# Kernel optimization log

Measured on AMD Instinct MI355X. Metric: run time of the kernel, lower is better.

Reference implementation:

```python
import jax, jax.numpy as jnp
import numpy as np

B, N, D = 16, 512, 256   # batch, tokens(=input_size), emb_dim
H, DH = 8, 16            # heads, dim_head
INNER = H * DH           # 128
SCALE = DH ** -0.5
EPS = 1e-5


def _p(key, shape):
    return jax.random.normal(key, shape, dtype=jnp.float32) * 0.02


def setup_inputs() -> dict:
    key = jax.random.key(0)
    ks = jax.random.split(key, 12)
    inp = {
        "x": jax.random.normal(ks[0], (B, N, D), dtype=jnp.float32),
        # stage-1 attention (tokens=N, feat=D)
        "wqkv1": _p(ks[1], (D, 3 * INNER)),
        "wo1": _p(ks[2], (INNER, D)),
        "bo1": jnp.zeros((D,), jnp.float32),
        "ff1_w1": _p(ks[3], (D, 8 * D)),
        "ff1_b1": jnp.zeros((8 * D,), jnp.float32),
        "ff1_w2": _p(ks[4], (4 * D, D)),
        "ff1_b2": jnp.zeros((D,), jnp.float32),
        # stage-2 attention (tokens=D after transpose, feat=N=input_size)
        "wqkv2": _p(ks[5], (N, 3 * INNER)),
        "wo2": _p(ks[6], (INNER, N)),
        "bo2": jnp.zeros((N,), jnp.float32),
        "ff2_w1": _p(ks[7], (N, 8 * N)),
        "ff2_b1": jnp.zeros((8 * N,), jnp.float32),
        "ff2_w2": _p(ks[8], (4 * N, N)),
        "ff2_b2": jnp.zeros((N,), jnp.float32),
        # layernorms
        "ln1_g": jnp.ones((D,), jnp.float32), "ln1_b": jnp.zeros((D,), jnp.float32),
        "ln2_g": jnp.ones((D,), jnp.float32), "ln2_b": jnp.zeros((D,), jnp.float32),
        "ln3_g": jnp.ones((N,), jnp.float32), "ln3_b": jnp.zeros((N,), jnp.float32),
        "ln4_g": jnp.ones((N,), jnp.float32), "ln4_b": jnp.zeros((N,), jnp.float32),
    }
    return inp


def _layernorm(x, g, b):
    mu = jnp.mean(x, axis=-1, keepdims=True)
    var = jnp.mean(jnp.square(x - mu), axis=-1, keepdims=True)
    return (x - mu) * jax.lax.rsqrt(var + EPS) * g + b


def _attention(x, wqkv, wo, bo, share):
    b, n, _ = x.shape
    qkv = x @ wqkv                                 # [b, n, 3*INNER]
    q, k, v = jnp.split(qkv, 3, axis=-1)
    split_heads = lambda t: t.reshape(b, n, H, DH).transpose(0, 2, 1, 3)
    q, k, v = split_heads(q), split_heads(k), split_heads(v)
    energy = jnp.einsum('bhid,bhjd->bhij', q, k) * SCALE
    if share is not None:
        energy = energy + share
    attn = jax.nn.softmax(energy, axis=-1)
    out = jnp.einsum('bhij,bhjd->bhid', attn, v)   # [b, h, n, dh]
    out = out.transpose(0, 2, 1, 3).reshape(b, n, INNER)
    return out @ wo + bo, energy


def _geglu_ff(x, w1, b1, w2, b2):
    h = x @ w1 + b1
    a, g = jnp.split(h, 2, axis=-1)
    return (a * jax.nn.gelu(g, approximate=False)) @ w2 + b2


def reference(x, wqkv1, wo1, bo1, ff1_w1, ff1_b1, ff1_w2, ff1_b2,
              wqkv2, wo2, bo2, ff2_w1, ff2_b1, ff2_w2, ff2_b2,
              ln1_g, ln1_b, ln2_g, ln2_b, ln3_g, ln3_b, ln4_g, ln4_b):
    # stage 1: token attention + FFN
    attn_out, share = _attention(x, wqkv1, wo1, bo1, None)
    x = _layernorm(attn_out + x, ln1_g, ln1_b)
    x = _layernorm(_geglu_ff(x, ff1_w1, ff1_b1, ff1_w2, ff1_b2) + x, ln2_g, ln2_b)
    # stage 2: feature (column) attention + FFN on transposed x
    x = x.transpose(0, 2, 1)                       # [b, D, N]
    attn_out, share2 = _attention(x, wqkv2, wo2, bo2, None)
    x = _layernorm(attn_out + x, ln3_g, ln3_b)
    x = _layernorm(_geglu_ff(x, ff2_w1, ff2_b1, ff2_w2, ff2_b2) + x, ln4_g, ln4_b)
    x = x.transpose(0, 2, 1)                       # [b, N, D]
    return (x, share, share2)
```

## Files before the change

kernel.cpp:

```cpp
#include <hip/hip_runtime.h>
#include <cstddef>


typedef __attribute__((ext_vector_type(8))) short short8;
typedef __attribute__((ext_vector_type(4))) short bf16x4;
typedef __attribute__((ext_vector_type(4))) float f32x4;
typedef unsigned short u16t;

__device__ __forceinline__ u16t f2b(float f) {
  union { float f; unsigned u; } x; x.f = f;
  unsigned r = (x.u + 0x7fffu + ((x.u >> 16) & 1u)) >> 16;
  return (u16t)r;
}

__device__ __forceinline__ void gload16(const void* g, void* l) {
  __builtin_amdgcn_global_load_lds(
      (const __attribute__((address_space(1))) void*)g,
      (__attribute__((address_space(3))) void*)l, 16, 0, 0);
}

__device__ __forceinline__ float gelu_f(float g) {
  const float x = g * 0.70710678118654752f;
  const float ax = fabsf(x);
  const float t = 1.f / (1.f + 0.3275911f * ax);
  const float p = t * (0.254829592f + t * (-0.284496736f +
                  t * (1.421413741f + t * (-1.453152027f + t * 1.061405429f))));
  const float er = 1.f - p * __expf(-x * x);
  return 0.5f * g * (1.f + copysignf(er, x));
}

__device__ __forceinline__ int origcol(int n, int halfN) {
  const int nb = n >> 7, s = (n >> 4) & 7, r = n & 15;
  return ((s & 1) ? halfN : 0) + (nb << 6) + ((s >> 1) << 4) + r;
}

template<int EPI>
__global__ __launch_bounds__(256) void mgemm(
    const u16t* __restrict__ A, const u16t* __restrict__ BT,
    const float* __restrict__ bias, const float* __restrict__ res,
    void* __restrict__ C, int M, int N, int K) {
  __shared__ u16t Al[128 * 32];
  __shared__ u16t Bl[128 * 32];
  const int t = threadIdx.x, lane = t & 63, wid = t >> 6;
  const int wr = wid >> 1, wc = wid & 1;
  const int lr = lane & 15, lq = lane >> 4;
  const int bm = blockIdx.y << 7, bn = blockIdx.x << 7;

  const int ao0 = wid * 2048 + lane * 16;
  const int ar0 = ao0 >> 6,          ac0 = (ao0 & 63) >> 1;
  const int ar1 = (ao0 + 1024) >> 6, ac1 = ((ao0 + 1024) & 63) >> 1;

  const u16t* Ab = A + (size_t)bm * K;
  const u16t* Bb = BT + (size_t)bn * K;

  f32x4 acc[4][4];
#pragma unroll
  for (int m = 0; m < 4; ++m)
#pragma unroll
    for (int n = 0; n < 4; ++n) acc[m][n] = (f32x4){0.f, 0.f, 0.f, 0.f};

  for (int k0 = 0; k0 < K; k0 += 32) {
    gload16(Ab + (size_t)ar0 * K + k0 + ac0, (char*)Al + wid * 2048);
    gload16(Ab + (size_t)ar1 * K + k0 + ac1, (char*)Al + wid * 2048 + 1024);
    gload16(Bb + (size_t)ar0 * K + k0 + ac0, (char*)Bl + wid * 2048);
    gload16(Bb + (size_t)ar1 * K + k0 + ac1, (char*)Bl + wid * 2048 + 1024);
    __syncthreads();
    short8 af[4], bf[4];
#pragma unroll
    for (int m = 0; m < 4; ++m)
      af[m] = *(const short8*)&Al[(wr * 64 + m * 16 + lr) * 32 + lq * 8];
#pragma unroll
    for (int n = 0; n < 4; ++n)
      bf[n] = *(const short8*)&Bl[(wc * 64 + n * 16 + lr) * 32 + lq * 8];
#pragma unroll
    for (int m = 0; m < 4; ++m)
#pragma unroll
      for (int n = 0; n < 4; ++n)
        acc[m][n] = __builtin_amdgcn_mfma_f32_16x16x32_bf16(af[m], bf[n], acc[m][n], 0, 0, 0);
    __syncthreads();
  }

  if (EPI == 2) {
    const int Nh = N >> 1;
#pragma unroll
    for (int np = 0; np < 2; ++np) {
      const int ca = bn + wc * 64 + np * 32 + lr;
      const float ba = bias[ca], bg = bias[ca + 16];
      const int uc = (bn >> 1) + wc * 32 + np * 16 + lr;
#pragma unroll
      for (int m = 0; m < 4; ++m) {
#pragma unroll
        for (int i = 0; i < 4; ++i) {
          const int row = bm + wr * 64 + m * 16 + lq * 4 + i;
          const float a = acc[m][2 * np][i] + ba;
          const float g = acc[m][2 * np + 1][i] + bg;
          ((u16t*)C)[(size_t)row * Nh + uc] = f2b(a * gelu_f(g));
        }
      }
    }
  } else {
#pragma unroll
    for (int n = 0; n < 4; ++n) {
      const int col = bn + wc * 64 + n * 16 + lr;
      const float bv = bias ? bias[col] : 0.f;
#pragma unroll
      for (int m = 0; m < 4; ++m) {
#pragma unroll
        for (int i = 0; i < 4; ++i) {
          const int row = bm + wr * 64 + m * 16 + lq * 4 + i;
          float v = acc[m][n][i] + bv;
          if (EPI == 1) {
            v += res[(size_t)row * N + col];
            ((float*)C)[(size_t)row * N + col] = v;
          } else {
            ((u16t*)C)[(size_t)row * N + col] = f2b(v);
          }
        }
      }
    }
  }
}

template<int EPI>
__global__ __launch_bounds__(256) void mgemm64(
    const u16t* __restrict__ A, const u16t* __restrict__ BT,
    const float* __restrict__ bias, const float* __restrict__ res,
    void* __restrict__ C, int M, int N, int K) {
  __shared__ u16t Al[64 * 32];
  __shared__ u16t Bl[64 * 32];
  const int t = threadIdx.x, lane = t & 63, wid = t >> 6;
  const int wr = wid >> 1, wc = wid & 1;
  const int lr = lane & 15, lq = lane >> 4;
  const int bm = blockIdx.y << 6, bn = blockIdx.x << 6;
  const int ch = wid * 64 + lane;
  const int crow = ch >> 2, ccol = (ch & 3) << 3;

  const u16t* Ab = A + (size_t)bm * K;
  const u16t* Bb = BT + (size_t)bn * K;

  f32x4 acc[2][2];
#pragma unroll
  for (int m = 0; m < 2; ++m)
#pragma unroll
    for (int n = 0; n < 2; ++n) acc[m][n] = (f32x4){0.f, 0.f, 0.f, 0.f};

  for (int k0 = 0; k0 < K; k0 += 32) {
    gload16(Ab + (size_t)crow * K + k0 + ccol, (char*)Al + wid * 1024);
    gload16(Bb + (size_t)crow * K + k0 + ccol, (char*)Bl + wid * 1024);
    __syncthreads();
    short8 af[2], bf[2];
#pragma unroll
    for (int m = 0; m < 2; ++m)
      af[m] = *(const short8*)&Al[(wr * 32 + m * 16 + lr) * 32 + lq * 8];
#pragma unroll
    for (int n = 0; n < 2; ++n)
      bf[n] = *(const short8*)&Bl[(wc * 32 + n * 16 + lr) * 32 + lq * 8];
#pragma unroll
    for (int m = 0; m < 2; ++m)
#pragma unroll
      for (int n = 0; n < 2; ++n)
        acc[m][n] = __builtin_amdgcn_mfma_f32_16x16x32_bf16(af[m], bf[n], acc[m][n], 0, 0, 0);
    __syncthreads();
  }

#pragma unroll
  for (int n = 0; n < 2; ++n) {
    const int col = bn + wc * 32 + n * 16 + lr;
    const float bv = bias ? bias[col] : 0.f;
#pragma unroll
    for (int m = 0; m < 2; ++m) {
#pragma unroll
      for (int i = 0; i < 4; ++i) {
        const int row = bm + wr * 32 + m * 16 + lq * 4 + i;
        float v = acc[m][n][i] + bv;
        if (EPI == 1) {
          v += res[(size_t)row * N + col];
          ((float*)C)[(size_t)row * N + col] = v;
        } else {
          ((u16t*)C)[(size_t)row * N + col] = f2b(v);
        }
      }
    }
  }
}

template<int NTOK>
__global__ __launch_bounds__(256) void attn_mfma(
    const u16t* __restrict__ qkv, float* __restrict__ share,
    u16t* __restrict__ outb) {
  __shared__ u16t VT[16][NTOK + 40];
  __shared__ u16t PB[4][16][40];
  const int t = threadIdx.x, lane = t & 63, wv = t >> 6;
  const int lr = lane & 15, lq = lane >> 4;
  const int bpb = NTOK / 64;
  const int bh = blockIdx.x / bpb, rg = blockIdx.x % bpb;
  const int b = bh >> 3, h = bh & 7;
  const u16t* qkvb = qkv + (size_t)b * NTOK * 384;

  for (int tok = t; tok < NTOK; tok += 256) {
    const u16t* vp = qkvb + (size_t)tok * 384 + 256 + h * 16;
    short8 v0 = *(const short8*)vp;
    short8 v1 = *(const short8*)(vp + 8);
#pragma unroll
    for (int d = 0; d < 8; ++d) {
      VT[d][tok]     = (u16t)v0[d];
      VT[d + 8][tok] = (u16t)v1[d];
    }
  }
  __syncthreads();

  const int i0 = rg * 64 + wv * 16;
  short8 qf = {0, 0, 0, 0, 0, 0, 0, 0};
  if (lq < 2)
    qf = *(const short8*)(qkvb + (size_t)(i0 + lr) * 384 + h * 16 + lq * 8);

  f32x4 oacc = {0.f, 0.f, 0.f, 0.f};
  f32x4 sacc = {0.f, 0.f, 0.f, 0.f};
  const f32x4 zero = {0.f, 0.f, 0.f, 0.f};
  float* shb = share + (size_t)bh * NTOK * NTOK;

  for (int t0 = 0; t0 < NTOK; t0 += 32) {
#pragma unroll
    for (int s2 = 0; s2 < 2; ++s2) {
      short8 kf = {0, 0, 0, 0, 0, 0, 0, 0};
      if (lq < 2)
        kf = *(const short8*)(qkvb + (size_t)(t0 + s2 * 16 + lr) * 384 + 128 + h * 16 + lq * 8);
      f32x4 e = __builtin_amdgcn_mfma_f32_16x16x32_bf16(qf, kf, zero, 0, 0, 0);
#pragma unroll
      for (int i = 0; i < 4; ++i) {
        const float ev = e[i] * 0.25f;
        shb[(size_t)(i0 + lq * 4 + i) * NTOK + t0 + s2 * 16 + lr] = ev;
        const float p = __expf(ev);
        sacc[i] += p;
        PB[wv][lq * 4 + i][s2 * 16 + lr] = f2b(p);
      }
    }
    asm volatile("s_waitcnt lgkmcnt(0)" ::: "memory");
    __builtin_amdgcn_sched_barrier(0);
    short8 pa = *(const short8*)&PB[wv][lr][lq * 8];
    short8 vf = *(const short8*)&VT[lr][t0 + lq * 8];
    oacc = __builtin_amdgcn_mfma_f32_16x16x32_bf16(pa, vf, oacc, 0, 0, 0);
    __builtin_amdgcn_sched_barrier(0);
  }
#pragma unroll
  for (int i = 0; i < 4; ++i) {
    float s = sacc[i];
    s += __shfl_xor(s, 1); s += __shfl_xor(s, 2);
    s += __shfl_xor(s, 4); s += __shfl_xor(s, 8);
    sacc[i] = s;
  }
#pragma unroll
  for (int i = 0; i < 4; ++i) {
    const float o = oacc[i] / sacc[i];
    outb[((size_t)(b * NTOK) + i0 + lq * 4 + i) * 128 + h * 16 + lr] = f2b(o);
  }
}

template<int NT, bool B16>
__global__ __launch_bounds__(NT) void ln_vec(
    const float* __restrict__ xin, const float* __restrict__ g,
    const float* __restrict__ be, float* __restrict__ y32,
    u16t* __restrict__ y16, int D) {
  const int row = blockIdx.x, t = threadIdx.x;
  const int lane = t & 63;
  const float4 x = ((const float4*)xin)[(size_t)row * (D >> 2) + t];
  float s = x.x + x.y + x.z + x.w;
  float s2 = x.x * x.x + x.y * x.y + x.z * x.z + x.w * x.w;
#pragma unroll
  for (int off = 32; off; off >>= 1) {
    s  += __shfl_xor(s, off);
    s2 += __shfl_xor(s2, off);
  }
  if (NT == 128) {
    __shared__ float a1[2], a2[2];
    const int wv = t >> 6;
    if (lane == 0) { a1[wv] = s; a2[wv] = s2; }
    __syncthreads();
    s = a1[0] + a1[1]; s2 = a2[0] + a2[1];
  }
  const float mean = s / D;
  const float var  = s2 / D - mean * mean;
  const float rstd = rsqrtf(var + 1e-5f);
  const float4 gv = ((const float4*)g)[t];
  const float4 bv = ((const float4*)be)[t];
  float4 y;
  y.x = (x.x - mean) * rstd * gv.x + bv.x;
  y.y = (x.y - mean) * rstd * gv.y + bv.y;
  y.z = (x.z - mean) * rstd * gv.z + bv.z;
  y.w = (x.w - mean) * rstd * gv.w + bv.w;
  ((float4*)y32)[(size_t)row * (D >> 2) + t] = y;
  if (B16) {
    bf16x4 p;
    p[0] = (short)f2b(y.x); p[1] = (short)f2b(y.y);
    p[2] = (short)f2b(y.z); p[3] = (short)f2b(y.w);
    *(bf16x4*)&y16[(size_t)row * D + t * 4] = p;
  }
}

template<bool BF16OUT>
__global__ void transp(const float* __restrict__ in, float* __restrict__ out32,
                       u16t* __restrict__ out16, int R, int C) {
  __shared__ float tile[32][33];
  const int b = blockIdx.z;
  const int r0 = blockIdx.y << 5, c0 = blockIdx.x << 5;
  const float* inb = in + (size_t)b * R * C;
  const int tx = threadIdx.x, ty = threadIdx.y;
#pragma unroll
  for (int dy = 0; dy < 32; dy += 8)
    tile[ty + dy][tx] = inb[(size_t)(r0 + ty + dy) * C + c0 + tx];
  __syncthreads();
#pragma unroll
  for (int dy = 0; dy < 32; dy += 8) {
    const float v = tile[tx][ty + dy];
    const size_t idx = (size_t)b * R * C + (size_t)(c0 + ty + dy) * R + r0 + tx;
    out32[idx] = v;
    if (BF16OUT) out16[idx] = f2b(v);
  }
}

__global__ __launch_bounds__(256) void prep_all(
    const float* __restrict__ x0, u16t* __restrict__ x16,
    const float* __restrict__ wqkv1, u16t* __restrict__ tqkv1,
    const float* __restrict__ wo1,   u16t* __restrict__ two1,
    const float* __restrict__ ff1w1, u16t* __restrict__ tff1a,
    const float* __restrict__ ff1w2, u16t* __restrict__ tff1b,
    const float* __restrict__ wqkv2, u16t* __restrict__ tqkv2,
    const float* __restrict__ wo2,   u16t* __restrict__ two2,
    const float* __restrict__ ff2w1, u16t* __restrict__ tff2a,
    const float* __restrict__ ff2w2, u16t* __restrict__ tff2b,
    const float* __restrict__ ff1b1, float* __restrict__ bp1,
    const float* __restrict__ ff2b1, float* __restrict__ bp2) {
  __shared__ float tile[32][33];
  const int b = blockIdx.x, t = threadIdx.x;
  const int tx = t & 31, ty = t >> 5;
  const float* src; u16t* dst;
  int K, N, bxd, blk, halfN = 0; bool perm = false;
  if (b < 1024) {
    const float* p = x0 + (size_t)(b * 256 + t) * 8;
    short8 v;
#pragma unroll
    for (int j = 0; j < 8; ++j) v[j] = (short)f2b(p[j]);
    *(short8*)(x16 + (size_t)(b * 256 + t) * 8) = v;
    return;
  } else if (b < 1120) { src = wqkv1; dst = tqkv1; K = 256;  N = 384;  bxd = 12;  blk = b - 1024; }
  else if (b < 1152)   { src = wo1;   dst = two1;  K = 128;  N = 256;  bxd = 8;   blk = b - 1120; }
  else if (b < 1664)   { src = ff1w1; dst = tff1a; K = 256;  N = 2048; bxd = 64;  blk = b - 1152; perm = true; halfN = 1024; }
  else if (b < 1920)   { src = ff1w2; dst = tff1b; K = 1024; N = 256;  bxd = 8;   blk = b - 1664; }
  else if (b < 2112)   { src = wqkv2; dst = tqkv2; K = 512;  N = 384;  bxd = 12;  blk = b - 1920; }
  else if (b < 2176)   { src = wo2;   dst = two2;  K = 128;  N = 512;  bxd = 16;  blk = b - 2112; }
  else if (b < 4224)   { src = ff2w1; dst = tff2a; K = 512;  N = 4096; bxd = 128; blk = b - 2176; perm = true; halfN = 2048; }
  else if (b < 5248)   { src = ff2w2; dst = tff2b; K = 2048; N = 512;  bxd = 16;  blk = b - 4224; }
  else if (b < 5256) { const int n = (b - 5248) * 256 + t; bp1[n] = ff1b1[origcol(n, 1024)]; return; }
  else               { const int n = (b - 5256) * 256 + t; bp2[n] = ff2b1[origcol(n, 2048)]; return; }

  const int bx = blk % bxd, by = blk / bxd;
  const int n0 = bx * 32, k0 = by * 32;
  const int nn = n0 + tx;
  const int no = perm ? origcol(nn, halfN) : nn;
#pragma unroll
  for (int dy = 0; dy < 32; dy += 8)
    tile[ty + dy][tx] = src[(size_t)(k0 + ty + dy) * N + no];
  __syncthreads();
#pragma unroll
  for (int dy = 0; dy < 32; dy += 8)
    dst[(size_t)(n0 + ty + dy) * K + k0 + tx] = f2b(tile[tx][ty + dy]);
}

extern "C" void kernel_launch(void* const* d_in, const int* in_sizes, int n_in,
                              void* d_out, int out_size, void* d_ws, size_t ws_size,
                              hipStream_t stream) {
  (void)in_sizes; (void)n_in; (void)out_size; (void)ws_size;
  const float* x0    = (const float*)d_in[0];
  const float* wqkv1 = (const float*)d_in[1];
  const float* wo1   = (const float*)d_in[2];
  const float* bo1   = (const float*)d_in[3];
  const float* ff1w1 = (const float*)d_in[4];
  const float* ff1b1 = (const float*)d_in[5];
  const float* ff1w2 = (const float*)d_in[6];
  const float* ff1b2 = (const float*)d_in[7];
  const float* wqkv2 = (const float*)d_in[8];
  const float* wo2   = (const float*)d_in[9];
  const float* bo2   = (const float*)d_in[10];
  const float* ff2w1 = (const float*)d_in[11];
  const float* ff2b1 = (const float*)d_in[12];
  const float* ff2w2 = (const float*)d_in[13];
  const float* ff2b2 = (const float*)d_in[14];
  const float* ln1g  = (const float*)d_in[15];
  const float* ln1b  = (const float*)d_in[16];
  const float* ln2g  = (const float*)d_in[17];
  const float* ln2b  = (const float*)d_in[18];
  const float* ln3g  = (const float*)d_in[19];
  const float* ln3b  = (const float*)d_in[20];
  const float* ln4g  = (const float*)d_in[21];
  const float* ln4b  = (const float*)d_in[22];

  float* out_x  = (float*)d_out;
  float* share1 = out_x + (size_t)2097152;
  float* share2 = share1 + (size_t)33554432;

  size_t off = 0;
  auto carve = [&](size_t bytes) -> void* {
    void* p = (char*)d_ws + off;
    off += (bytes + 255) & ~(size_t)255;
    return p;
  };
  u16t*  x16    = (u16t*)carve((size_t)8192 * 256 * 2);
  u16t*  qkv16  = (u16t*)carve((size_t)8192 * 384 * 2);
  u16t*  attn16 = (u16t*)carve((size_t)8192 * 128 * 2);
  float* sumb   = (float*)carve((size_t)8192 * 256 * 4);
  float* xa32   = (float*)carve((size_t)8192 * 256 * 4);
  u16t*  xa16   = (u16t*)carve((size_t)8192 * 256 * 2);
  float* xb32   = (float*)carve((size_t)8192 * 256 * 4);
  float* xt32   = (float*)carve((size_t)8192 * 256 * 4);
  u16t*  xt16   = (u16t*)carve((size_t)8192 * 256 * 2);
  float* xc32   = (float*)carve((size_t)8192 * 256 * 4);
  u16t*  xc16   = (u16t*)carve((size_t)8192 * 256 * 2);
  float* xd32   = (float*)carve((size_t)8192 * 256 * 4);
  u16t*  ubuf   = (u16t*)carve((size_t)8192 * 1024 * 2);
  u16t*  tqkv1  = (u16t*)carve((size_t)384 * 256 * 2);
  u16t*  two1   = (u16t*)carve((size_t)256 * 128 * 2);
  u16t*  tff1a  = (u16t*)carve((size_t)2048 * 256 * 2);
  u16t*  tff1b  = (u16t*)carve((size_t)256 * 1024 * 2);
  u16t*  tqkv2  = (u16t*)carve((size_t)384 * 512 * 2);
  u16t*  two2   = (u16t*)carve((size_t)512 * 128 * 2);
  u16t*  tff2a  = (u16t*)carve((size_t)4096 * 512 * 2);
  u16t*  tff2b  = (u16t*)carve((size_t)512 * 2048 * 2);
  float* bp1    = (float*)carve((size_t)2048 * 4);
  float* bp2    = (float*)carve((size_t)4096 * 4);

  prep_all<<<5272, 256, 0, stream>>>(x0, x16, wqkv1, tqkv1, wo1, two1,
      ff1w1, tff1a, ff1w2, tff1b, wqkv2, tqkv2, wo2, two2,
      ff2w1, tff2a, ff2w2, tff2b, ff1b1, bp1, ff2b1, bp2);

  mgemm64<0><<<dim3(6, 128), 256, 0, stream>>>(x16, tqkv1, nullptr, nullptr, qkv16, 8192, 384, 256);
  attn_mfma<512><<<1024, 256, 0, stream>>>(qkv16, share1, attn16);
  mgemm64<1><<<dim3(4, 128), 256, 0, stream>>>(attn16, two1, bo1, x0, sumb, 8192, 256, 128);
  ln_vec<64, true><<<8192, 64, 0, stream>>>(sumb, ln1g, ln1b, xa32, xa16, 256);
  mgemm<2><<<dim3(16, 64), 256, 0, stream>>>(xa16, tff1a, bp1, nullptr, ubuf, 8192, 2048, 256);
  mgemm64<1><<<dim3(4, 128), 256, 0, stream>>>(ubuf, tff1b, ff1b2, xa32, sumb, 8192, 256, 1024);
  ln_vec<64, false><<<8192, 64, 0, stream>>>(sumb, ln2g, ln2b, xb32, nullptr, 256);

  transp<true><<<dim3(8, 16, 16), dim3(32, 8), 0, stream>>>(xb32, xt32, xt16, 512, 256);

  mgemm64<0><<<dim3(6, 64), 256, 0, stream>>>(xt16, tqkv2, nullptr, nullptr, qkv16, 4096, 384, 512);
  attn_mfma<256><<<512, 256, 0, stream>>>(qkv16, share2, attn16);
  mgemm64<1><<<dim3(8, 64), 256, 0, stream>>>(attn16, two2, bo2, xt32, sumb, 4096, 512, 128);
  ln_vec<128, true><<<4096, 128, 0, stream>>>(sumb, ln3g, ln3b, xc32, xc16, 512);
  mgemm<2><<<dim3(32, 32), 256, 0, stream>>>(xc16, tff2a, bp2, nullptr, ubuf, 4096, 4096, 512);
  mgemm64<1><<<dim3(8, 64), 256, 0, stream>>>(ubuf, tff2b, ff2b2, xc32, sumb, 4096, 512, 2048);
  ln_vec<128, false><<<4096, 128, 0, stream>>>(sumb, ln4g, ln4b, xd32, nullptr, 512);

  transp<false><<<dim3(16, 8, 16), dim3(32, 8), 0, stream>>>(xd32, out_x, nullptr, 256, 512);
}
```

Baseline: 215.6 us.

## Fuse attention output projection with residual add and LayerNorm

Adds a gemmlnF kernel in which each block computes a 32-row strip of the full output width for the K=128 output projection. It adds bias and residual, then computes the LayerNorm row statistics through shuffles and shared memory, and writes fp32 and bf16 results. This replaces the separate mgemm64 and ln_vec launches for both stages and removes the intermediate sum buffer round trip. In exchange it uses only 256 or 128 blocks with large dynamic LDS (the full weight matrix per block), which lowers parallelism and occupancy. It also uses a single-pass variance formula.

Result: no change. 215.7 us (+0.0%).

```diff
diff --git a/kernel.cpp b/kernel.cpp
--- a/kernel.cpp
+++ b/kernel.cpp
@@ -182,6 +182,113 @@
       }
     }
   }
+}
+
+template<int NW>
+__global__ __launch_bounds__(256) void gemmlnF(
+    const u16t* __restrict__ A, const u16t* __restrict__ BT,
+    const float* __restrict__ bias, const float* __restrict__ res,
+    const float* __restrict__ g, const float* __restrict__ be,
+    float* __restrict__ y32, u16t* __restrict__ y16) {
+  constexpr int NR = NW / 64;
+  extern __shared__ u16t lds[];
+  u16t* Al = lds;
+  u16t* Bl = lds + 32 * 128;
+  __shared__ float psum[4][32], psq[4][32];
+  const int t = threadIdx.x, lane = t & 63, wid = t >> 6;
+  const int lr = lane & 15, lq = lane >> 4;
+  const int bm = blockIdx.x << 5;
+  const int wofs = wid * (NW / 4);
+
+  const int c0 = wid * 64 + lane;
+#pragma unroll
+  for (int j = 0; j < 2; ++j) {
+    const int c = j * 256 + c0;
+    gload16(A + (size_t)(bm + (c >> 4)) * 128 + ((c & 15) << 3),
+            (char*)Al + (size_t)(j * 256 + wid * 64) * 16);
+  }
+#pragma unroll
+  for (int j = 0; j < NW / 16; ++j) {
+    const int c = j * 256 + c0;
+    gload16(BT + (size_t)(c >> 4) * 128 + ((c & 15) << 3),
+            (char*)Bl + (size_t)(j * 256 + wid * 64) * 16);
+  }
+  __syncthreads();
+
+  f32x4 acc[2][NR];
+#pragma unroll
+  for (int m = 0; m < 2; ++m)
+#pragma unroll
+    for (int n = 0; n < NR; ++n) acc[m][n] = (f32x4){0.f, 0.f, 0.f, 0.f};
+
+#pragma unroll
+  for (int kk = 0; kk < 4; ++kk) {
+    short8 af[2], bf[NR];
+#pragma unroll
+    for (int m = 0; m < 2; ++m)
+      af[m] = *(const short8*)&Al[(m * 16 + lr) * 128 + kk * 32 + lq * 8];
+#pragma unroll
+    for (int n = 0; n < NR; ++n)
+      bf[n] = *(const short8*)&Bl[(wofs + n * 16 + lr) * 128 + kk * 32 + lq * 8];
+#pragma unroll
+    for (int m = 0; m < 2; ++m)
+#pragma unroll
+      for (int n = 0; n < NR; ++n)
+        acc[m][n] = __builtin_amdgcn_mfma_f32_16x16x32_bf16(af[m], bf[n], acc[m][n], 0, 0, 0);
+  }
+
+  float ps[2][4], ps2[2][4];
+#pragma unroll
+  for (int m = 0; m < 2; ++m)
+#pragma unroll
+    for (int i = 0; i < 4; ++i) { ps[m][i] = 0.f; ps2[m][i] = 0.f; }
+#pragma unroll
+  for (int m = 0; m < 2; ++m)
+#pragma unroll
+    for (int n = 0; n < NR; ++n) {
+      const int col = wofs + n * 16 + lr;
+      const float bv = bias[col];
+#pragma unroll
+      for (int i = 0; i < 4; ++i) {
+        const int row = bm + m * 16 + lq * 4 + i;
+        const float v = acc[m][n][i] + bv + res[(size_t)row * NW + col];
+        acc[m][n][i] = v;
+        ps[m][i] += v; ps2[m][i] += v * v;
+      }
+    }
+#pragma unroll
+  for (int m = 0; m < 2; ++m)
+#pragma unroll
+    for (int i = 0; i < 4; ++i) {
+      float s = ps[m][i], s2 = ps2[m][i];
+      s  += __shfl_xor(s, 1);  s  += __shfl_xor(s, 2);
+      s  += __shfl_xor(s, 4);  s  += __shfl_xor(s, 8);
+      s2 += __shfl_xor(s2, 1); s2 += __shfl_xor(s2, 2);
+      s2 += __shfl_xor(s2, 4); s2 += __shfl_xor(s2, 8);
+      if (lr == 0) {
+        psum[wid][m * 16 + lq * 4 + i] = s;
+        psq[wid][m * 16 + lq * 4 + i]  = s2;
+      }
+    }
+  __syncthreads();
+#pragma unroll
+  for (int m = 0; m < 2; ++m)
+#pragma unroll
+    for (int i = 0; i < 4; ++i) {
+      const int r = m * 16 + lq * 4 + i;
+      const float tot = psum[0][r] + psum[1][r] + psum[2][r] + psum[3][r];
+      const float tq  = psq[0][r]  + psq[1][r]  + psq[2][r]  + psq[3][r];
+      const float mean = tot / NW;
+      const float rstd = rsqrtf(tq / NW - mean * mean + 1e-5f);
+      const int row = bm + r;
+#pragma unroll
+      for (int n = 0; n < NR; ++n) {
+        const int col = wofs + n * 16 + lr;
+        const float y = (acc[m][n][i] - mean) * rstd * g[col] + be[col];
+        y32[(size_t)row * NW + col] = y;
+        y16[(size_t)row * NW + col] = f2b(y);
+      }
+    }
 }
 
 template<int NTOK>
@@ -428,14 +535,18 @@
   float* bp1    = (float*)carve((size_t)2048 * 4);
   float* bp2    = (float*)carve((size_t)4096 * 4);
 
+  (void)hipFuncSetAttribute(reinterpret_cast<const void*>(&gemmlnF<256>),
+                            hipFuncAttributeMaxDynamicSharedMemorySize, 73728);
+  (void)hipFuncSetAttribute(reinterpret_cast<const void*>(&gemmlnF<512>),
+                            hipFuncAttributeMaxDynamicSharedMemorySize, 139264);
+
   prep_all<<<5272, 256, 0, stream>>>(x0, x16, wqkv1, tqkv1, wo1, two1,
       ff1w1, tff1a, ff1w2, tff1b, wqkv2, tqkv2, wo2, two2,
       ff2w1, tff2a, ff2w2, tff2b, ff1b1, bp1, ff2b1, bp2);
 
   mgemm64<0><<<dim3(6, 128), 256, 0, stream>>>(x16, tqkv1, nullptr, nullptr, qkv16, 8192, 384, 256);
   attn_mfma<512><<<1024, 256, 0, stream>>>(qkv16, share1, attn16);
-  mgemm64<1><<<dim3(4, 128), 256, 0, stream>>>(attn16, two1, bo1, x0, sumb, 8192, 256, 128);
-  ln_vec<64, true><<<8192, 64, 0, stream>>>(sumb, ln1g, ln1b, xa32, xa16, 256);
+  gemmlnF<256><<<256, 256, 73728, stream>>>(attn16, two1, bo1, x0, ln1g, ln1b, xa32, xa16);
   mgemm<2><<<dim3(16, 64), 256, 0, stream>>>(xa16, tff1a, bp1, nullptr, ubuf, 8192, 2048, 256);
   mgemm64<1><<<dim3(4, 128), 256, 0, stream>>>(ubuf, tff1b, ff1b2, xa32, sumb, 8192, 256, 1024);
   ln_vec<64, false><<<8192, 64, 0, stream>>>(sumb, ln2g, ln2b, xb32, nullptr, 256);
@@ -444,8 +555,7 @@
 
   mgemm64<0><<<dim3(6, 64), 256, 0, stream>>>(xt16, tqkv2, nullptr, nullptr, qkv16, 4096, 384, 512);
   attn_mfma<256><<<512, 256, 0, stream>>>(qkv16, share2, attn16);
-  mgemm64<1><<<dim3(8, 64), 256, 0, stream>>>(attn16, two2, bo2, xt32, sumb, 4096, 512, 128);
-  ln_vec<128, true><<<4096, 128, 0, stream>>>(sumb, ln3g, ln3b, xc32, xc16, 512);
+  gemmlnF<512><<<128, 256, 139264, stream>>>(attn16, two2, bo2, xt32, ln3g, ln3b, xc32, xc16);
   mgemm<2><<<dim3(32, 32), 256, 0, stream>>>(xc16, tff2a, bp2, nullptr, ubuf, 4096, 4096, 512);
   mgemm64<1><<<dim3(8, 64), 256, 0, stream>>>(ubuf, tff2b, ff2b2, xc32, sumb, 4096, 512, 2048);
   ln_vec<128, false><<<4096, 128, 0, stream>>>(sumb, ln4g, ln4b, xd32, nullptr, 512);
```
